# Optimization experiments

Measured on AMD Instinct MI355X. Metric: run time of the kernel, lower is better.

The kernel has to match this reference:

```python
import jax, jax.numpy as jnp
import numpy as np

B, L, D, V, NL, K = 2, 2048, 512, 50257, 12, 5
A = D // 4   # active recurrence channels
H = D // 4   # LowRankFF hidden (reduction_factor=4)
EPS = 1e-6


def rmsnorm(x, w):
    rms = jnp.sqrt(jnp.mean(x * x, axis=-1, keepdims=True) + EPS)
    return w * (x / rms)


def rope(x):
    # x: [B, L, D]
    half = D // 2
    inv_freq = 1.0 / (10000.0 ** (jnp.arange(half, dtype=jnp.float32) / half))
    freqs = jnp.arange(x.shape[1], dtype=jnp.float32)[:, None] * inv_freq[None, :]  # [L, half]
    emb = jnp.concatenate([freqs, freqs], axis=-1)  # [L, D]
    cos, sin = jnp.cos(emb)[None], jnp.sin(emb)[None]
    x1, x2 = x[..., :half], x[..., half:]
    rot = jnp.concatenate([-x2, x1], axis=-1)
    return x * cos + rot * sin


def recurrence(x, alpha, beta):
    # diagonal linear recurrence on first A channels: h = alpha*h + beta*x_t
    xa = jnp.swapaxes(x[..., :A], 0, 1)  # [L, B, A]
    def step(h, xt):
        h = alpha * h + beta * xt
        return h, h
    _, hs = jax.lax.scan(step, jnp.zeros((x.shape[0], A), x.dtype), xa)
    hs = jnp.swapaxes(hs, 0, 1)  # [B, L, A]
    return jnp.concatenate([hs, x[..., A:]], axis=-1)


def block(x, p, dil):
    (nw, dw, db, pw, pb, al, be, w1, b1, w2, b2, dnw, dnb, upw, upb) = p
    residual = x
    xn = rmsnorm(x, nw)
    # depthwise conv (groups=D), 'same' length since pad = 2*dil
    xc = jnp.swapaxes(xn, 1, 2)  # [B, D, L]
    pad = (K - 1) * dil // 2
    xc = jax.lax.conv_general_dilated(
        xc, dw.reshape(D, 1, K), window_strides=(1,), padding=[(pad, pad)],
        rhs_dilation=(dil,), dimension_numbers=('NCH', 'OIH', 'NCH'),
        feature_group_count=D) + db[None, :, None]
    # pointwise conv (1x1)
    xc = jnp.einsum('bdl,ed->ble', xc, pw) + pb
    xr = recurrence(xn, al, be)
    x = xc + xr
    # gated fusion
    g1 = jnp.einsum('bld,od->blo', x, w1) + b1
    g2 = jnp.einsum('bld,od->blo', x, w2) + b2
    x = x + jax.nn.sigmoid(g1) * jnp.tanh(g2)
    # low-rank FF
    hdn = jax.nn.gelu(jnp.einsum('bld,hd->blh', x, dnw) + dnb, approximate=False)
    x = x + jnp.einsum('blh,dh->bld', hdn, upw) + upb
    return x + residual


def setup_inputs() -> dict:
    key = jax.random.key(0)
    ks = jax.random.split(key, 10)
    s = 0.02
    f32 = jnp.float32
    return {
        'tokens': jax.random.randint(ks[0], (B, L), 0, V, dtype=jnp.int32),
        'emb': (jax.random.normal(ks[1], (V, D)) * s).astype(f32),
        'norm_w': jnp.ones((NL, D), f32),
        'dconv_w': (jax.random.normal(ks[2], (NL, D, K)) * 0.1).astype(f32),
        'dconv_b': jnp.zeros((NL, D), f32),
        'pconv_w': (jax.random.normal(ks[3], (NL, D, D)) * s).astype(f32),
        'pconv_b': jnp.zeros((NL, D), f32),
        'alpha': jnp.full((NL, A), 0.9, f32),
        'beta': jnp.full((NL, A), 0.1, f32),
        'w1': (jax.random.normal(ks[4], (NL, D, D)) * s).astype(f32),
        'b1': jnp.zeros((NL, D), f32),
        'w2': (jax.random.normal(ks[5], (NL, D, D)) * s).astype(f32),
        'b2': jnp.zeros((NL, D), f32),
        'down_w': (jax.random.normal(ks[6], (NL, H, D)) * s).astype(f32),
        'down_b': jnp.zeros((NL, H), f32),
        'up_w': (jax.random.normal(ks[7], (NL, D, H)) * s).astype(f32),
        'up_b': jnp.zeros((NL, D), f32),
        'final_norm_w': jnp.ones((D,), f32),
    }


def reference(tokens, emb, norm_w, dconv_w, dconv_b, pconv_w, pconv_b, alpha, beta,
              w1, b1, w2, b2, down_w, down_b, up_w, up_b, final_norm_w):
    x = emb[tokens]           # [B, L, D]
    x = rope(x)
    for i in range(NL):
        dil = 2 ** (i % 3)
        p = (norm_w[i], dconv_w[i], dconv_b[i], pconv_w[i], pconv_b[i],
             alpha[i], beta[i], w1[i], b1[i], w2[i], b2[i],
             down_w[i], down_b[i], up_w[i], up_b[i])
        x = block(x, p, dil)
    x = rmsnorm(x, final_norm_w)
    logits = jnp.einsum('bld,vd->blv', x, emb)  # tied output projection
    return logits
```

## Files before the change

### kernel.cpp

```cpp
#include <hip/hip_runtime.h>

#define DEV __device__ __forceinline__

constexpr int Bb = 2, Ls = 2048, Dd = 512, Vv = 50257, NLl = 12, Kk = 5;
constexpr int Aa = Dd / 4;
constexpr int Hh = Dd / 4;
constexpr int Mm = Bb * Ls;
constexpr float EPSf = 1e-6f;
constexpr int NC = 64, Lc = Ls / NC;

typedef __bf16 bf16x8 __attribute__((ext_vector_type(8)));
typedef float f32x4 __attribute__((ext_vector_type(4)));

typedef __attribute__((address_space(1))) void GVoid;
typedef __attribute__((address_space(3))) void LVoid;

DEV void gl_lds16(const void* g, void* l) {
  __builtin_amdgcn_global_load_lds((GVoid*)g, (LVoid*)l, 16, 0, 0);
}

DEV unsigned short f2bf(float f) {
  unsigned u = __builtin_bit_cast(unsigned, f);
  u += 0x7fffu + ((u >> 16) & 1u);
  return (unsigned short)(u >> 16);
}

struct CvtArgs {
  const float* src[6];
  unsigned short* dst[6];
  int n4[6];
};

__global__ __launch_bounds__(256) void k_cvt_multi(CvtArgs a, int total4) {
  int i = blockIdx.x * 256 + threadIdx.x;
  if (i >= total4) return;
#pragma unroll
  for (int s = 0; s < 6; s++) {
    if (i < a.n4[s]) {
      float4 v = ((const float4*)a.src[s])[i];
      ushort4 o;
      o.x = f2bf(v.x); o.y = f2bf(v.y); o.z = f2bf(v.z); o.w = f2bf(v.w);
      ((ushort4*)a.dst[s])[i] = o;
      return;
    }
    i -= a.n4[s];
  }
}

__global__ __launch_bounds__(256) void k_embed(const int* __restrict__ tok,
                                               const float* __restrict__ emb,
                                               float* __restrict__ X) {
  int m = blockIdx.x;
  int l = m & (Ls - 1);
  int t = tok[m];
  const float* er = emb + (size_t)t * Dd;
  int d = threadIdx.x;
  float inv = powf(10000.f, -(float)d * (1.f / 256.f));
  float ang = (float)l * inv;
  float s, c;
  sincosf(ang, &s, &c);
  float x1 = er[d], x2 = er[d + 256];
  X[(size_t)m * Dd + d]       = x1 * c - x2 * s;
  X[(size_t)m * Dd + d + 256] = x2 * c + x1 * s;
}

template <bool BF16OUT>
__global__ __launch_bounds__(256) void k_rms(const float* __restrict__ X,
                                             const float* __restrict__ w,
                                             float* __restrict__ outF,
                                             unsigned short* __restrict__ outB) {
  int m = blockIdx.x;
  const float* xr = X + (size_t)m * Dd;
  int t = threadIdx.x;
  float2 v = ((const float2*)xr)[t];
  float ss = v.x * v.x + v.y * v.y;
  for (int off = 32; off; off >>= 1) ss += __shfl_down(ss, off, 64);
  __shared__ float red[4];
  int lane = t & 63, wid = t >> 6;
  if (!lane) red[wid] = ss;
  __syncthreads();
  float tot = red[0] + red[1] + red[2] + red[3];
  float inv = rsqrtf(tot * (1.f / Dd) + EPSf);
  float2 wv = ((const float2*)w)[t];
  float o0 = wv.x * v.x * inv, o1 = wv.y * v.y * inv;
  if (BF16OUT) {
    ushort2 uv; uv.x = f2bf(o0); uv.y = f2bf(o1);
    ((ushort2*)(outB + (size_t)m * Dd))[t] = uv;
  } else {
    float2 ov; ov.x = o0; ov.y = o1;
    ((float2*)(outF + (size_t)m * Dd))[t] = ov;
  }
}

__global__ __launch_bounds__(256) void k_dwconv(const float* __restrict__ XN,
                                                const float* __restrict__ w,
                                                const float* __restrict__ bias,
                                                unsigned short* __restrict__ CB, int dil) {
  int idx = blockIdx.x * 256 + threadIdx.x;
  int d = idx & (Dd - 1);
  int ml = idx >> 9;
  int l = ml & (Ls - 1);
  float acc = bias[d];
#pragma unroll
  for (int k = 0; k < 5; k++) {
    int ll = l + (k - 2) * dil;
    if (ll >= 0 && ll < Ls) acc += w[d * 5 + k] * XN[(size_t)(ml + (ll - l)) * Dd + d];
  }
  CB[idx] = f2bf(acc);
}

__global__ __launch_bounds__(128) void k_scanA(const float* __restrict__ XN,
                                               const float* __restrict__ al,
                                               const float* __restrict__ be,
                                               float* __restrict__ X2, float* __restrict__ S) {
  int b = blockIdx.x >> 6, c = blockIdx.x & 63;
  int a = threadIdx.x;
  float av = al[a], bv = be[a], h = 0.f;
  size_t base = ((size_t)b * Ls + c * Lc) * Dd + a;
#pragma unroll 4
  for (int j = 0; j < Lc; j++) {
    float xv = XN[base + (size_t)j * Dd];
    h = av * h + bv * xv;
    X2[base + (size_t)j * Dd] = h;
  }
  S[(b * NC + c) * Aa + a] = h;
}

__global__ __launch_bounds__(256) void k_scanB(const float* __restrict__ al,
                                               const float* __restrict__ S,
                                               float* __restrict__ Cin,
                                               float* __restrict__ alP) {
  int t = threadIdx.x;
  int b = t >> 7, a = t & 127;
  float av = al[a];
  float pw = 1.f;
#pragma unroll
  for (int j = 0; j < Lc; j++) {
    pw *= av;
    if (b == 0) alP[a * Lc + j] = pw;
  }
  float aL = pw;
  float carry = 0.f;
  for (int c = 0; c < NC; c++) {
    Cin[(b * NC + c) * Aa + a] = carry;
    carry = aL * carry + S[(b * NC + c) * Aa + a];
  }
}

enum : int { EPI_PCONV = 0, EPI_GATE = 1, EPI_GELU = 2, EPI_UP = 3, EPI_OUT = 4 };

template <int BM, int BN, int EPI, bool DUALB, bool MASKN, bool SWAP>
__global__ __launch_bounds__(256) void k_gemm(const unsigned short* __restrict__ A,
                                              const unsigned short* __restrict__ B1,
                                              const unsigned short* __restrict__ B2,
                                              const float* __restrict__ bias1,
                                              const float* __restrict__ bias2,
                                              const float* __restrict__ add1,
                                              const float* __restrict__ add2,
                                              const float* __restrict__ aux1,
                                              const float* __restrict__ aux2,
                                              float* __restrict__ outF,
                                              unsigned short* __restrict__ outB,
                                              int K, int ldc, int nmax) {
  constexpr int NB = DUALB ? 2 : 1;
  __shared__ unsigned short smem[BM * 64 + NB * BN * 64];
  unsigned short* smA = smem;
  unsigned short* smB1 = smem + BM * 64;
  unsigned short* smB2 = smB1 + (DUALB ? BN * 64 : 0);

  const int tid = threadIdx.x, lane = tid & 63, wid = tid >> 6;
  const int bm = (SWAP ? blockIdx.x : blockIdx.y) * BM;
  const int bn = (SWAP ? blockIdx.y : blockIdx.x) * BN;
  constexpr int TM = BM / 32, TN = BN / 32;
  const int wm = (wid & 1) * (BM / 2), wn = (wid >> 1) * (BN / 2);
  const int q = lane >> 4, mr = lane & 15;

  f32x4 acc1[TM][TN] = {};
  f32x4 acc2[TM][TN] = {};

  for (int kb = 0; kb < K; kb += 64) {
#pragma unroll
    for (int bch = 0; bch < BM * 8 / 256; ++bch) {
      int s = bch * 256 + wid * 64 + lane;
      int r = s >> 3, c = (s & 7) ^ (r & 7);
      gl_lds16(A + (size_t)(bm + r) * K + kb + c * 8, smA + (size_t)(bch * 256 + wid * 64) * 8);
    }
#pragma unroll
    for (int bch = 0; bch < BN * 8 / 256; ++bch) {
      int s = bch * 256 + wid * 64 + lane;
      int r = s >> 3, c = (s & 7) ^ (r & 7);
      int row = bn + r;
      if (MASKN) row = min(row, nmax - 1);
      gl_lds16(B1 + (size_t)row * K + kb + c * 8, smB1 + (size_t)(bch * 256 + wid * 64) * 8);
      if constexpr (DUALB)
        gl_lds16(B2 + (size_t)row * K + kb + c * 8, smB2 + (size_t)(bch * 256 + wid * 64) * 8);
    }
    __syncthreads();
#pragma unroll
    for (int ks = 0; ks < 2; ++ks) {
      bf16x8 af[TM], bfa[TN], bfb[TN];
#pragma unroll
      for (int i = 0; i < TM; i++) {
        int r = wm + i * 16 + mr, c = ks * 4 + q;
        af[i] = *(const bf16x8*)(smA + (r * 8 + (c ^ (r & 7))) * 8);
      }
#pragma unroll
      for (int j = 0; j < TN; j++) {
        int r = wn + j * 16 + mr, c = ks * 4 + q;
        int slot = r * 8 + (c ^ (r & 7));
        bfa[j] = *(const bf16x8*)(smB1 + slot * 8);
        if constexpr (DUALB) bfb[j] = *(const bf16x8*)(smB2 + slot * 8);
      }
#pragma unroll
      for (int i = 0; i < TM; i++)
#pragma unroll
        for (int j = 0; j < TN; j++) {
          acc1[i][j] = __builtin_amdgcn_mfma_f32_16x16x32_bf16(af[i], bfa[j], acc1[i][j], 0, 0, 0);
          if constexpr (DUALB)
            acc2[i][j] = __builtin_amdgcn_mfma_f32_16x16x32_bf16(af[i], bfb[j], acc2[i][j], 0, 0, 0);
        }
    }
    __syncthreads();
  }

#pragma unroll
  for (int i = 0; i < TM; i++) {
#pragma unroll
    for (int j = 0; j < TN; j++) {
      int col = bn + wn + j * 16 + mr;
      if (MASKN && col >= nmax) continue;
#pragma unroll
      for (int r = 0; r < 4; r++) {
        int row = bm + wm + i * 16 + q * 4 + r;
        size_t o = (size_t)row * ldc + col;
        float a1 = acc1[i][j][r];
        if constexpr (EPI == EPI_OUT) {
          outF[o] = a1;
        } else if constexpr (EPI == EPI_PCONV) {
          float y = a1 + bias1[col];
          float v;
          if (col < Aa) {
            int l = row & (Ls - 1);
            int b = row >> 11;
            int jj = l & (Lc - 1), c = l >> 5;
            float h = add1[o] + aux2[col * Lc + jj] * aux1[(b * NC + c) * Aa + col];
            v = y + h;
          } else {
            v = y + add2[o];
          }
          outF[o] = v;
          outB[o] = f2bf(v);
        } else if constexpr (EPI == EPI_GELU) {
          float g = a1 + bias1[col];
          float h = 0.5f * g * (1.f + erff(g * 0.70710678118654752f));
          outB[o] = f2bf(h);
        } else if constexpr (EPI == EPI_GATE) {
          float g1 = a1 + bias1[col];
          float g2 = acc2[i][j][r] + bias2[col];
          float sg = 1.f / (1.f + expf(-g1));
          float v = add1[o] + sg * tanhf(g2);
          outF[o] = v;
          outB[o] = f2bf(v);
        } else if constexpr (EPI == EPI_UP) {
          float v = a1 + bias1[col] + add1[o] + add2[o];
          outF[o] = v;
        }
      }
    }
  }
}

extern "C" void kernel_launch(void* const* d_in, const int* in_sizes, int n_in,
                              void* d_out, int out_size, void* d_ws, size_t ws_size,
                              hipStream_t stream) {
  const int*   tokens  = (const int*)d_in[0];
  const float* emb     = (const float*)d_in[1];
  const float* norm_w  = (const float*)d_in[2];
  const float* dconv_w = (const float*)d_in[3];
  const float* dconv_b = (const float*)d_in[4];
  const float* pconv_w = (const float*)d_in[5];
  const float* pconv_b = (const float*)d_in[6];
  const float* alpha   = (const float*)d_in[7];
  const float* beta    = (const float*)d_in[8];
  const float* w1      = (const float*)d_in[9];
  const float* b1      = (const float*)d_in[10];
  const float* w2      = (const float*)d_in[11];
  const float* b2      = (const float*)d_in[12];
  const float* down_w  = (const float*)d_in[13];
  const float* down_b  = (const float*)d_in[14];
  const float* up_w    = (const float*)d_in[15];
  const float* up_b    = (const float*)d_in[16];
  const float* fnw     = (const float*)d_in[17];
  float* out = (float*)d_out;

  char* p = (char*)d_ws;
  auto alloc = [&](size_t bytes) {
    void* r = p;
    p += (bytes + 255) & ~(size_t)255;
    return r;
  };
  float* X   = (float*)alloc((size_t)Mm * Dd * 4);
  float* XN  = (float*)alloc((size_t)Mm * Dd * 4);
  float* X2  = (float*)alloc((size_t)Mm * Dd * 4);
  float* X3  = (float*)alloc((size_t)Mm * Dd * 4);
  unsigned short* CB  = (unsigned short*)alloc((size_t)Mm * Dd * 2);
  unsigned short* X2B = (unsigned short*)alloc((size_t)Mm * Dd * 2);
  unsigned short* X3B = (unsigned short*)alloc((size_t)Mm * Dd * 2);
  unsigned short* XFB = (unsigned short*)alloc((size_t)Mm * Dd * 2);
  unsigned short* HB  = (unsigned short*)alloc((size_t)Mm * Hh * 2);
  float* S   = (float*)alloc((size_t)Bb * NC * Aa * 4);
  float* Cin = (float*)alloc((size_t)Bb * NC * Aa * 4);
  float* alP = (float*)alloc((size_t)Aa * Lc * 4);
  unsigned short* embB = (unsigned short*)alloc((size_t)Vv * Dd * 2);
  unsigned short* pwB  = (unsigned short*)alloc((size_t)NLl * Dd * Dd * 2);
  unsigned short* w1B  = (unsigned short*)alloc((size_t)NLl * Dd * Dd * 2);
  unsigned short* w2B  = (unsigned short*)alloc((size_t)NLl * Dd * Dd * 2);
  unsigned short* dwB  = (unsigned short*)alloc((size_t)NLl * Hh * Dd * 2);
  unsigned short* upB  = (unsigned short*)alloc((size_t)NLl * Dd * Hh * 2);

  CvtArgs ca;
  ca.src[0] = emb;     ca.dst[0] = embB; ca.n4[0] = (Vv * Dd) / 4;
  ca.src[1] = pconv_w; ca.dst[1] = pwB;  ca.n4[1] = (NLl * Dd * Dd) / 4;
  ca.src[2] = w1;      ca.dst[2] = w1B;  ca.n4[2] = (NLl * Dd * Dd) / 4;
  ca.src[3] = w2;      ca.dst[3] = w2B;  ca.n4[3] = (NLl * Dd * Dd) / 4;
  ca.src[4] = down_w;  ca.dst[4] = dwB;  ca.n4[4] = (NLl * Hh * Dd) / 4;
  ca.src[5] = up_w;    ca.dst[5] = upB;  ca.n4[5] = (NLl * Dd * Hh) / 4;
  int total4 = ca.n4[0] + ca.n4[1] + ca.n4[2] + ca.n4[3] + ca.n4[4] + ca.n4[5];
  k_cvt_multi<<<(total4 + 255) / 256, 256, 0, stream>>>(ca, total4);

  k_embed<<<Mm, 256, 0, stream>>>(tokens, emb, X);

  for (int i = 0; i < NLl; i++) {
    int dil = 1 << (i % 3);
    k_rms<false><<<Mm, 256, 0, stream>>>(X, norm_w + i * Dd, XN, nullptr);
    k_dwconv<<<Mm * Dd / 256, 256, 0, stream>>>(XN, dconv_w + (size_t)i * Dd * Kk,
                                                dconv_b + i * Dd, CB, dil);
    k_scanA<<<Bb * NC, 128, 0, stream>>>(XN, alpha + i * Aa, beta + i * Aa, X2, S);
    k_scanB<<<1, 256, 0, stream>>>(alpha + i * Aa, S, Cin, alP);
    k_gemm<64, 64, EPI_PCONV, false, false, false><<<dim3(8, 64), 256, 0, stream>>>(
        CB, pwB + (size_t)i * Dd * Dd, nullptr, pconv_b + i * Dd, nullptr,
        X2, XN, Cin, alP, X2, X2B, Dd, Dd, 0);
    k_gemm<64, 64, EPI_GATE, true, false, false><<<dim3(8, 64), 256, 0, stream>>>(
        X2B, w1B + (size_t)i * Dd * Dd, w2B + (size_t)i * Dd * Dd, b1 + i * Dd, b2 + i * Dd,
        X2, nullptr, nullptr, nullptr, X3, X3B, Dd, Dd, 0);
    k_gemm<32, 64, EPI_GELU, false, false, false><<<dim3(2, 128), 256, 0, stream>>>(
        X3B, dwB + (size_t)i * Hh * Dd, nullptr, down_b + i * Hh, nullptr,
        nullptr, nullptr, nullptr, nullptr, nullptr, HB, Dd, Hh, 0);
    k_gemm<64, 64, EPI_UP, false, false, false><<<dim3(8, 64), 256, 0, stream>>>(
        HB, upB + (size_t)i * Dd * Hh, nullptr, up_b + i * Dd, nullptr,
        X3, X, nullptr, nullptr, X, nullptr, Hh, Dd, 0);
  }

  k_rms<true><<<Mm, 256, 0, stream>>>(X, fnw, nullptr, XFB);
  k_gemm<128, 128, EPI_OUT, false, true, true><<<dim3(Mm / 128, (Vv + 127) / 128), 256, 0, stream>>>(
      XFB, embB, nullptr, nullptr, nullptr, nullptr, nullptr, nullptr, nullptr,
      out, nullptr, Dd, Vv, Vv);
}
```

Before: 2.146 ms.

## Double-buffer GEMM LDS tiles and add a 256x256 tile kernel for logits

Adds double-buffered LDS staging to the generic GEMM. Loads for tile t+2 are issued while tile t is computed, using explicit vmcnt waits, barriers and MFMA priority raising in place of a full sync after each tile. Adds a dedicated 512-thread 256x256 tile kernel for the tied output projection, to raise data reuse and overlap on the largest GEMM. The cost is doubled shared memory use, which lowers occupancy, and fragile hand-written vmcnt counting.

```diff
diff --git a/kernel.cpp b/kernel.cpp
--- a/kernel.cpp
+++ b/kernel.cpp
@@ -18,6 +18,17 @@
 DEV void gl_lds16(const void* g, void* l) {
   __builtin_amdgcn_global_load_lds((GVoid*)g, (LVoid*)l, 16, 0, 0);
 }
+
+template <int N> DEV void waitvm() {
+  if constexpr (N == 0) asm volatile("s_waitcnt vmcnt(0)" ::: "memory");
+  else if constexpr (N == 3) asm volatile("s_waitcnt vmcnt(3)" ::: "memory");
+  else if constexpr (N == 4) asm volatile("s_waitcnt vmcnt(4)" ::: "memory");
+  else if constexpr (N == 6) asm volatile("s_waitcnt vmcnt(6)" ::: "memory");
+  else if constexpr (N == 8) asm volatile("s_waitcnt vmcnt(8)" ::: "memory");
+  else static_assert(N == 0, "unsupported vmcnt");
+}
+DEV void sbar() { __builtin_amdgcn_s_barrier(); }
+DEV void schedb() { __builtin_amdgcn_sched_barrier(0); }
 
 DEV unsigned short f2bf(float f) {
   unsigned u = __builtin_bit_cast(unsigned, f);
@@ -163,10 +174,10 @@
                                               unsigned short* __restrict__ outB,
                                               int K, int ldc, int nmax) {
   constexpr int NB = DUALB ? 2 : 1;
-  __shared__ unsigned short smem[BM * 64 + NB * BN * 64];
-  unsigned short* smA = smem;
-  unsigned short* smB1 = smem + BM * 64;
-  unsigned short* smB2 = smB1 + (DUALB ? BN * 64 : 0);
+  constexpr int TILE = (BM + NB * BN) * 64;
+  constexpr int ARND = BM * 8 / 256, BRND = BN * 8 / 256;
+  constexpr int NLD = ARND + NB * BRND;
+  __shared__ unsigned short smem[2 * TILE];
 
   const int tid = threadIdx.x, lane = tid & 63, wid = tid >> 6;
   const int bm = (SWAP ? blockIdx.x : blockIdx.y) * BM;
@@ -178,15 +189,20 @@
   f32x4 acc1[TM][TN] = {};
   f32x4 acc2[TM][TN] = {};
 
-  for (int kb = 0; kb < K; kb += 64) {
-#pragma unroll
-    for (int bch = 0; bch < BM * 8 / 256; ++bch) {
+  const int NT = K >> 6;
+
+  auto stage = [&](int kb, int buf) {
+    unsigned short* smA = smem + buf * TILE;
+    unsigned short* smB1 = smA + BM * 64;
+    unsigned short* smB2 = DUALB ? smB1 + BN * 64 : smB1;
+#pragma unroll
+    for (int bch = 0; bch < ARND; ++bch) {
       int s = bch * 256 + wid * 64 + lane;
       int r = s >> 3, c = (s & 7) ^ (r & 7);
       gl_lds16(A + (size_t)(bm + r) * K + kb + c * 8, smA + (size_t)(bch * 256 + wid * 64) * 8);
     }
 #pragma unroll
-    for (int bch = 0; bch < BN * 8 / 256; ++bch) {
+    for (int bch = 0; bch < BRND; ++bch) {
       int s = bch * 256 + wid * 64 + lane;
       int r = s >> 3, c = (s & 7) ^ (r & 7);
       int row = bn + r;
@@ -195,7 +211,18 @@
       if constexpr (DUALB)
         gl_lds16(B2 + (size_t)row * K + kb + c * 8, smB2 + (size_t)(bch * 256 + wid * 64) * 8);
     }
-    __syncthreads();
+  };
+
+  stage(0, 0);
+  stage(64, 1);
+  waitvm<NLD>();
+  sbar();
+  schedb();
+
+  for (int t = 0;; ++t) {
+    const unsigned short* smA = smem + (t & 1) * TILE;
+    const unsigned short* smB1 = smA + BM * 64;
+    const unsigned short* smB2 = DUALB ? smB1 + BN * 64 : smB1;
 #pragma unroll
     for (int ks = 0; ks < 2; ++ks) {
       bf16x8 af[TM], bfa[TN], bfb[TN];
@@ -211,6 +238,7 @@
         bfa[j] = *(const bf16x8*)(smB1 + slot * 8);
         if constexpr (DUALB) bfb[j] = *(const bf16x8*)(smB2 + slot * 8);
       }
+      __builtin_amdgcn_s_setprio(1);
 #pragma unroll
       for (int i = 0; i < TM; i++)
 #pragma unroll
@@ -219,8 +247,19 @@
           if constexpr (DUALB)
             acc2[i][j] = __builtin_amdgcn_mfma_f32_16x16x32_bf16(af[i], bfb[j], acc2[i][j], 0, 0, 0);
         }
-    }
-    __syncthreads();
+      __builtin_amdgcn_s_setprio(0);
+    }
+    if (t == NT - 1) break;
+    schedb();
+    sbar();
+    if (t + 2 < NT) {
+      stage((t + 2) * 64, t & 1);
+      waitvm<NLD>();
+    } else {
+      waitvm<0>();
+    }
+    sbar();
+    schedb();
   }
 
 #pragma unroll
@@ -270,6 +309,94 @@
   }
 }
 
+__global__ __launch_bounds__(512, 2) void k_gemm256(const unsigned short* __restrict__ A,
+                                                    const unsigned short* __restrict__ B,
+                                                    float* __restrict__ out,
+                                                    int K, int nmax) {
+  constexpr int TILE = 2 * 256 * 64;
+  __shared__ unsigned short smem[2 * TILE];
+  const int tid = threadIdx.x, lane = tid & 63, wid = tid >> 6;
+  const int bm = blockIdx.x * 256, bn = blockIdx.y * 256;
+  const int wm = (wid >> 2) * 128, wn = (wid & 3) * 64;
+  const int q = lane >> 4, mr = lane & 15;
+
+  f32x4 acc[8][4] = {};
+  const int NT = K >> 6;
+
+  auto stage = [&](int kb, int buf) {
+    unsigned short* smA = smem + buf * TILE;
+    unsigned short* smB = smA + 256 * 64;
+#pragma unroll
+    for (int bch = 0; bch < 4; ++bch) {
+      int s = bch * 512 + wid * 64 + lane;
+      int r = s >> 3, c = (s & 7) ^ (r & 7);
+      gl_lds16(A + (size_t)(bm + r) * K + kb + c * 8, smA + (size_t)(bch * 512 + wid * 64) * 8);
+    }
+#pragma unroll
+    for (int bch = 0; bch < 4; ++bch) {
+      int s = bch * 512 + wid * 64 + lane;
+      int r = s >> 3, c = (s & 7) ^ (r & 7);
+      int row = min(bn + r, nmax - 1);
+      gl_lds16(B + (size_t)row * K + kb + c * 8, smB + (size_t)(bch * 512 + wid * 64) * 8);
+    }
+  };
+
+  stage(0, 0);
+  stage(64, 1);
+  waitvm<8>();
+  sbar();
+  schedb();
+
+  for (int t = 0;; ++t) {
+    const unsigned short* smA = smem + (t & 1) * TILE;
+    const unsigned short* smB = smA + 256 * 64;
+#pragma unroll
+    for (int ks = 0; ks < 2; ++ks) {
+      bf16x8 af[8], bf[4];
+#pragma unroll
+      for (int i = 0; i < 8; i++) {
+        int r = wm + i * 16 + mr, c = ks * 4 + q;
+        af[i] = *(const bf16x8*)(smA + (r * 8 + (c ^ (r & 7))) * 8);
+      }
+#pragma unroll
+      for (int j = 0; j < 4; j++) {
+        int r = wn + j * 16 + mr, c = ks * 4 + q;
+        bf[j] = *(const bf16x8*)(smB + (r * 8 + (c ^ (r & 7))) * 8);
+      }
+      __builtin_amdgcn_s_setprio(1);
+#pragma unroll
+      for (int i = 0; i < 8; i++)
+#pragma unroll
+        for (int j = 0; j < 4; j++)
+          acc[i][j] = __builtin_amdgcn_mfma_f32_16x16x32_bf16(af[i], bf[j], acc[i][j], 0, 0, 0);
+      __builtin_amdgcn_s_setprio(0);
+    }
+    if (t == NT - 1) break;
+    schedb();
+    sbar();
+    if (t + 2 < NT) {
+      stage((t + 2) * 64, t & 1);
+      waitvm<8>();
+    } else {
+      waitvm<0>();
+    }
+    sbar();
+    schedb();
+  }
+
+#pragma unroll
+  for (int i = 0; i < 8; i++) {
+#pragma unroll
+    for (int j = 0; j < 4; j++) {
+      int col = bn + wn + j * 16 + mr;
+      if (col >= nmax) continue;
+      size_t o = (size_t)(bm + wm + i * 16 + q * 4) * nmax + col;
+#pragma unroll
+      for (int r = 0; r < 4; r++) out[o + (size_t)r * nmax] = acc[i][j][r];
+    }
+  }
+}
+
 extern "C" void kernel_launch(void* const* d_in, const int* in_sizes, int n_in,
                               void* d_out, int out_size, void* d_ws, size_t ws_size,
                               hipStream_t stream) {
@@ -352,7 +479,5 @@
   }
 
   k_rms<true><<<Mm, 256, 0, stream>>>(X, fnw, nullptr, XFB);
-  k_gemm<128, 128, EPI_OUT, false, true, true><<<dim3(Mm / 128, (Vv + 127) / 128), 256, 0, stream>>>(
-      XFB, embB, nullptr, nullptr, nullptr, nullptr, nullptr, nullptr, nullptr,
-      out, nullptr, Dd, Vv, Vv);
-}
+  k_gemm256<<<dim3(Mm / 256, (Vv + 255) / 256), 512, 0, stream>>>(XFB, embB, out, Dd, Vv);
+}
```

New measurement: 2.008 ms. -6.4%, faster.
